# Kernel optimization log

Hardware: AMD Instinct MI355X
Metric: run time of the kernel (lower is better)

## Reference

```python
import jax, jax.numpy as jnp
import numpy as np

DIN = 1024
DOUT = 1024


def setup_inputs() -> dict:
    key = jax.random.key(0)
    kx, kq, kk, kv = jax.random.split(key, 4)
    B, T = 4, 2048
    x = jax.random.normal(kx, (B, T, DIN), dtype=jnp.float32)
    # nn.Linear weights are (dout, din); init like PyTorch default scale
    s = 1.0 / np.sqrt(DIN)
    Wq = jax.random.uniform(kq, (DOUT, DIN), minval=-s, maxval=s, dtype=jnp.float32)
    Wk = jax.random.uniform(kk, (DOUT, DIN), minval=-s, maxval=s, dtype=jnp.float32)
    Wv = jax.random.uniform(kv, (DOUT, DIN), minval=-s, maxval=s, dtype=jnp.float32)
    return {"x": x, "Wq": Wq, "Wk": Wk, "Wv": Wv}


def reference(x, Wq, Wk, Wv):
    B, T, _ = x.shape
    q = jnp.einsum('btd,ed->bte', x, Wq)
    k = jnp.einsum('btd,ed->bte', x, Wk)
    v = jnp.einsum('btd,ed->bte', x, Wv)
    attn = jnp.einsum('bqe,bke->bqk', q, k)  # [B, T, T]
    # Faithful to source: masked_fill result is discarded, so the causal mask
    # is a MULTIPLICATIVE tril of ones (upper triangle logits become 0, not -inf).
    mask = jnp.tril(jnp.ones((T, T), dtype=attn.dtype))
    attn = attn * mask
    # Faithful to source: scale by sqrt(last dim of attn) = sqrt(T), not sqrt(d).
    attn = jax.nn.softmax(attn / jnp.sqrt(jnp.asarray(T, attn.dtype)), axis=-1)
    return jnp.einsum('bqk,bke->bqe', attn, v)
```

## Files before the change

kernel.cpp:

```cpp
#include <hip/hip_runtime.h>
#include <stdint.h>

#define BB 4
#define TT 2048
#define DD 1024
#define NX (BB*TT*DD)
#define NW (DD*DD)
#define SCALE 0.022097086912079608f
#define SCALEI 2.157918643757774e-5f
#define UNSCALE 7.689469810104304e-6f
#define Q8F 2.4606299212598425e-4f
#define VQ 48.0f
#define PVF (1.0f/3072.0f)
#define TQF (1.0f/24.0f)

typedef short v8s __attribute__((ext_vector_type(8)));
typedef float v4f __attribute__((ext_vector_type(4)));
typedef int   v4i __attribute__((ext_vector_type(4)));
typedef uint8_t u8;

typedef const void __attribute__((address_space(1))) *as1_cvp;
typedef void __attribute__((address_space(3))) *as3_vp;

__device__ __forceinline__ short f2bf(float f) {
    union { float f; uint32_t u; } x; x.f = f;
    uint32_t r = x.u + 0x7fffu + ((x.u >> 16) & 1u);
    return (short)(r >> 16);
}
__device__ __forceinline__ float bf2f(short s) {
    union { uint32_t u; float f; } x; x.u = ((uint32_t)(uint16_t)s) << 16;
    return x.f;
}
__device__ __forceinline__ int bsum(uint32_t w) {
#if __has_builtin(__builtin_amdgcn_sdot4)
    return __builtin_amdgcn_sdot4((int)w, 0x01010101, 0, false);
#else
    return (int)(signed char)(w & 255) + (int)(signed char)((w >> 8) & 255) +
           (int)(signed char)((w >> 16) & 255) + (int)(signed char)((w >> 24) & 255);
#endif
}

__device__ __forceinline__ void gl_lds16(const void* g, const void* lds_wave_base) {
    __builtin_amdgcn_global_load_lds(
        (as1_cvp)(uintptr_t)g,
        (as3_vp)(uint32_t)(uintptr_t)lds_wave_base,
        16, 0, 0);
}

#define WAITV(N) asm volatile("s_waitcnt vmcnt(" #N ")" ::: "memory")

__device__ __forceinline__ void stage128B(const u8* __restrict__ g, int lda,
                                          u8* lds, int tid) {
    #pragma unroll
    for (int s = 0; s < 2; s++) {
        int t = s * 512 + tid;
        int r = t >> 3, c = t & 7, cg = c ^ (r & 7);
        gl_lds16(g + (size_t)r * lda + cg * 16, lds + s * 8192 + (tid >> 6) * 1024);
    }
}
__device__ __forceinline__ void stB8(const u8* __restrict__ g, u8* lds, int tid, int p) {
    #pragma unroll
    for (int s = 0; s < 2; s++) {
        int t = s * 512 + tid;
        int r = t >> 3, c = t & 7, cg = c ^ (r & 7);
        int grow = ((r >> 5) << 6) + p * 32 + (r & 31);
        gl_lds16(g + (size_t)grow * 1024 + cg * 16, lds + s * 8192 + (tid >> 6) * 1024);
    }
}
__device__ __forceinline__ v4i frag16(const u8* lds, int row, int c) {
    return *(const v4i*)(lds + row * 128 + ((c ^ (row & 7)) << 4));
}

__device__ __forceinline__ void stage64(const u8* __restrict__ g, u8* lds, int tid) {
    int r = tid >> 2, c = tid & 3;
    gl_lds16(g + (size_t)r * 1024 + c * 16, lds + (tid >> 6) * 1024);
}
__device__ __forceinline__ v4i fragK64(const u8* lds, int row, int gq) {
    return *(const v4i*)(lds + row * 64 + gq * 16);
}

__global__ void k_convert(const float* __restrict__ x, const float* __restrict__ Wq,
                          const float* __restrict__ Wk, const float* __restrict__ Wv,
                          u8* __restrict__ dst8, float* __restrict__ rowsum) {
    int i = blockIdx.x * 256 + threadIdx.x;
    if (i < BB * TT) rowsum[i] = (float)((15 - ((i & 2047) >> 7)) * 128);
    size_t base = (size_t)i * 4;
    const float* src; size_t off; float sc; bool clip;
    if (base < NX)               { src = x;  off = base; sc = 32.f; clip = true; }
    else if (base < NX + NW)     { src = Wq; off = base - NX; sc = 4064.f; clip = false; }
    else if (base < NX + 2*(size_t)NW) { src = Wk; off = base - NX - NW; sc = 4064.f; clip = false; }
    else                         { src = Wv; off = base - NX - 2*(size_t)NW; sc = 4064.f; clip = false; }
    float4 f = *(const float4*)(src + off);
    float a0 = f.x * sc, a1 = f.y * sc, a2 = f.z * sc, a3 = f.w * sc;
    if (clip) {
        a0 = fminf(fmaxf(a0, -127.f), 127.f);
        a1 = fminf(fmaxf(a1, -127.f), 127.f);
        a2 = fminf(fmaxf(a2, -127.f), 127.f);
        a3 = fminf(fmaxf(a3, -127.f), 127.f);
    }
    int q0 = __float2int_rn(a0), q1 = __float2int_rn(a1);
    int q2 = __float2int_rn(a2), q3 = __float2int_rn(a3);
    uint32_t w = (uint32_t)(q0 & 255) | ((uint32_t)(q1 & 255) << 8) |
                 ((uint32_t)(q2 & 255) << 16) | ((uint32_t)(q3 & 255) << 24);
    *(uint32_t*)(dst8 + base) = w;
}

__global__ __launch_bounds__(512, 2) void k_qkv(const u8* __restrict__ xb,
                                                const u8* __restrict__ wb,
                                                u8* __restrict__ q8,
                                                u8* __restrict__ k8,
                                                short* __restrict__ vt,
                                                u8* __restrict__ vt8) {
    int h = blockIdx.x;
    int w = (h & 7) * 96 + (h >> 3);
    int which = w >> 8, rem = w & 255, ntile = rem >> 6, mtile = rem & 63;
    int m0 = mtile * 128, n0 = ntile * 256;
    const u8* Ag = xb + (size_t)m0 * 1024;
    const u8* Bg = wb + (size_t)which * NW + (size_t)n0 * 1024;
    __shared__ __align__(16) u8 SH[98304];
    int tid = threadIdx.x, lane = tid & 63, wave = tid >> 6;
    int wm = wave >> 2, wn = wave & 3;
    int lr = lane & 15, lq = lane >> 4;
    int arow = wm * 64 + lr;
    int brow = wn * 32 + lr;
    v4i acc[4][4];
    #pragma unroll
    for (int i = 0; i < 4; i++)
        #pragma unroll
        for (int j = 0; j < 4; j++) acc[i][j] = (v4i){0, 0, 0, 0};

    stage128B(Ag, 1024, SH, tid);
    stB8(Bg, SH + 16384, tid, 0);
    stB8(Bg, SH + 32768, tid, 1);

    #pragma unroll
    for (int t = 0; t < 8; ++t) {
        u8* S  = SH + (t & 1) * 49152;
        u8* Sn = SH + ((t + 1) & 1) * 49152;
        const u8* Agn = Ag + (t + 1) * 128;
        const u8* Bgn = Bg + (t + 1) * 128;
        WAITV(2);
        __builtin_amdgcn_s_barrier();
        v4i af[4][2], bf[2][2];
        #pragma unroll
        for (int i = 0; i < 4; i++)
            #pragma unroll
            for (int kh = 0; kh < 2; kh++) af[i][kh] = frag16(S, arow + i * 16, kh * 4 + lq);
        #pragma unroll
        for (int jj = 0; jj < 2; jj++)
            #pragma unroll
            for (int kh = 0; kh < 2; kh++) bf[jj][kh] = frag16(S + 16384, brow + jj * 16, kh * 4 + lq);
        if (t < 7) {
            stage128B(Agn, 1024, Sn,  tid);
            stB8(Bgn, Sn + 16384, tid, 0);
        }
        __builtin_amdgcn_s_setprio(1);
        #pragma unroll
        for (int kh = 0; kh < 2; kh++)
            #pragma unroll
            for (int i = 0; i < 4; i++)
                #pragma unroll
                for (int jj = 0; jj < 2; jj++)
                    acc[i][jj] = __builtin_amdgcn_mfma_i32_16x16x64_i8(af[i][kh], bf[jj][kh], acc[i][jj], 0, 0, 0);
        __builtin_amdgcn_s_setprio(0);
        if (t < 7) { WAITV(4); }
        else       { WAITV(0); }
        __builtin_amdgcn_s_barrier();
        v4i bg2[2][2];
        #pragma unroll
        for (int jj = 0; jj < 2; jj++)
            #pragma unroll
            for (int kh = 0; kh < 2; kh++) bg2[jj][kh] = frag16(S + 32768, brow + jj * 16, kh * 4 + lq);
        if (t < 7) stB8(Bgn, Sn + 32768, tid, 1);
        __builtin_amdgcn_s_setprio(1);
        #pragma unroll
        for (int kh = 0; kh < 2; kh++)
            #pragma unroll
            for (int i = 0; i < 4; i++)
                #pragma unroll
                for (int jj = 0; jj < 2; jj++)
                    acc[i][2 + jj] = __builtin_amdgcn_mfma_i32_16x16x64_i8(af[i][kh], bg2[jj][kh], acc[i][2 + jj], 0, 0, 0);
        __builtin_amdgcn_s_setprio(0);
    }

    if (which == 2) {
        #pragma unroll
        for (int a = 0; a < 4; a++)
            #pragma unroll
            for (int b = 0; b < 4; b++) {
                int row0 = m0 + wm * 64 + a * 16 + lq * 4;
                int col  = n0 + wn * 64 + b * 16 + lr;
                int bb = row0 >> 11, tt0 = row0 & 2047;
                size_t idx = ((size_t)bb << 21) + ((size_t)col << 11) + tt0;
                float v0 = (float)acc[a][b][0] * UNSCALE;
                float v1 = (float)acc[a][b][1] * UNSCALE;
                float v2 = (float)acc[a][b][2] * UNSCALE;
                float v3 = (float)acc[a][b][3] * UNSCALE;
                short4 hv; hv.x = f2bf(v0); hv.y = f2bf(v1); hv.z = f2bf(v2); hv.w = f2bf(v3);
                *(short4*)(vt + idx) = hv;
                int c0 = __float2int_rn(fminf(fmaxf(v0 * VQ, -127.f), 127.f));
                int c1 = __float2int_rn(fminf(fmaxf(v1 * VQ, -127.f), 127.f));
                int c2 = __float2int_rn(fminf(fmaxf(v2 * VQ, -127.f), 127.f));
                int c3 = __float2int_rn(fminf(fmaxf(v3 * VQ, -127.f), 127.f));
                uint32_t pw = (uint32_t)(c0 & 255) | ((uint32_t)(c1 & 255) << 8) |
                              ((uint32_t)(c2 & 255) << 16) | ((uint32_t)(c3 & 255) << 24);
                *(uint32_t*)(vt8 + idx) = pw;
            }
    } else {
        u8* outp = (which == 0) ? q8 : k8;
        #pragma unroll
        for (int a = 0; a < 4; a++)
            #pragma unroll
            for (int b = 0; b < 4; b++)
                #pragma unroll
                for (int r = 0; r < 4; r++) {
                    int row = m0 + wm * 64 + a * 16 + lq * 4 + r;
                    int col = n0 + wn * 64 + b * 16 + lr;
                    float v = (float)acc[a][b][r] * Q8F;
                    v = fminf(fmaxf(v, -127.f), 127.f);
                    outp[(size_t)row * 1024 + col] = (u8)(__float2int_rn(v) & 255);
                }
    }
}

__global__ void k_ts1(const short* __restrict__ vt, const u8* __restrict__ vt8,
                      float* __restrict__ TSpart, float* __restrict__ TQpart) {
    int g = blockIdx.x * 256 + threadIdx.x;
    int b = g >> 14, jt = (g >> 10) & 15, e = g & 1023;
    const short* row = vt + ((size_t)b << 21) + ((size_t)e << 11) + jt * 128;
    float s = 0.f;
    #pragma unroll
    for (int c = 0; c < 16; c++) {
        uint4 u = *(const uint4*)(row + c * 8);
        const short* hp = (const short*)&u;
        #pragma unroll
        for (int z = 0; z < 8; z++) s += bf2f(hp[z]);
    }
    TSpart[g] = s;
    const u8* row8 = vt8 + ((size_t)b << 21) + ((size_t)e << 11) + jt * 128;
    int si = 0;
    #pragma unroll
    for (int c = 0; c < 8; c++) {
        uint4 u = *(const uint4*)(row8 + c * 16);
        si += bsum(u.x) + bsum(u.y) + bsum(u.z) + bsum(u.w);
    }
    TQpart[g] = (float)si;
}
__global__ void k_ts2(const float* __restrict__ TSpart, const float* __restrict__ TQpart,
                      float* __restrict__ TS, float* __restrict__ TQ) {
    int g = blockIdx.x * 256 + threadIdx.x;
    int b = g >> 10, e = g & 1023;
    float acc = 0.f;
    TS[(size_t)(b * 17 + 16) * 1024 + e] = 0.f;
    for (int jt = 15; jt >= 0; jt--) {
        acc += TSpart[(size_t)(b * 16 + jt) * 1024 + e];
        TS[(size_t)(b * 17 + jt) * 1024 + e] = acc;
    }
    float aq = 0.f;
    TQ[(size_t)(b * 17 + 0) * 1024 + e] = 0.f;
    for (int jt = 0; jt < 16; jt++) {
        aq += TQpart[(size_t)(b * 16 + jt) * 1024 + e];
        TQ[(size_t)(b * 17 + jt + 1) * 1024 + e] = aq;
    }
}

__global__ __launch_bounds__(512, 4) void k_pk(const u8* __restrict__ q8,
                                               const u8* __restrict__ k8,
                                               char* __restrict__ P8,
                                               float* __restrict__ rowsum) {
    int pidx = blockIdx.x, b = blockIdx.z;
    int qt = 0;
    while ((qt + 1) * (qt + 2) / 2 <= pidx) qt++;
    int kt = pidx - qt * (qt + 1) / 2;
    int r0 = qt * 128;
    const u8* Ag = q8 + ((size_t)b * 2048 + r0) * 1024;
    const u8* Bg = k8 + ((size_t)b * 2048 + (size_t)kt * 128) * 1024;
    __shared__ __align__(16) u8 SH[49152];
    int tid = threadIdx.x, lane = tid & 63, wave = tid >> 6;
    int wm2 = wave >> 2, wn4 = wave & 3;
    int lr = lane & 15, lq = lane >> 4;
    v4i acc[4][2];
    #pragma unroll
    for (int i = 0; i < 4; i++)
        #pragma unroll
        for (int j = 0; j < 2; j++) acc[i][j] = (v4i){0, 0, 0, 0};

    stage64(Ag,      SH,                tid);
    stage64(Bg,      SH + 8192,         tid);
    stage64(Ag + 64, SH + 16384,        tid);
    stage64(Bg + 64, SH + 16384 + 8192, tid);

    #pragma unroll
    for (int it = 0; it < 16; ++it) {
        if (it + 1 < 16) { WAITV(2); }
        else             { WAITV(0); }
        __builtin_amdgcn_s_barrier();
        if (it + 2 < 16) {
            u8* Sn = SH + ((it + 2) % 3) * 16384;
            stage64(Ag + (it + 2) * 64, Sn,        tid);
            stage64(Bg + (it + 2) * 64, Sn + 8192, tid);
        }
        const u8* S = SH + (it % 3) * 16384;
        v4i af[4], bf[2];
        #pragma unroll
        for (int i = 0; i < 4; i++) af[i] = fragK64(S, wm2 * 64 + i * 16 + lr, lq);
        #pragma unroll
        for (int j = 0; j < 2; j++) bf[j] = fragK64(S + 8192, wn4 * 32 + j * 16 + lr, lq);
        __builtin_amdgcn_s_setprio(1);
        #pragma unroll
        for (int i = 0; i < 4; i++)
            #pragma unroll
            for (int j = 0; j < 2; j++)
                acc[i][j] = __builtin_amdgcn_mfma_i32_16x16x64_i8(af[i], bf[j], acc[i][j], 0, 0, 0);
        __builtin_amdgcn_s_setprio(0);
    }
    char* Pb = P8 + ((size_t)b << 22);
    float rs[4][4];
    #pragma unroll
    for (int i = 0; i < 4; i++)
        #pragma unroll
        for (int r = 0; r < 4; r++) rs[i][r] = 0.f;
    #pragma unroll
    for (int i = 0; i < 4; i++)
        #pragma unroll
        for (int j = 0; j < 2; j++)
            #pragma unroll
            for (int r = 0; r < 4; r++) {
                int qi = r0 + wm2 * 64 + i * 16 + lq * 4 + r;
                int kj = kt * 128 + wn4 * 32 + j * 16 + lr;
                float p = (kj <= qi) ? __expf((float)acc[i][j][r] * SCALEI) : 1.0f;
                int u = __float2int_rn(fminf(p * 64.f, 255.f));
                Pb[(size_t)qi * 2048 + kj] = (char)(u - 128);
                rs[i][r] += (float)u * 0.015625f;
            }
    #pragma unroll
    for (int m = 1; m < 16; m <<= 1)
        #pragma unroll
        for (int i = 0; i < 4; i++)
            #pragma unroll
            for (int r = 0; r < 4; r++) rs[i][r] += __shfl_xor(rs[i][r], m);
    if (lr == 0)
        #pragma unroll
        for (int i = 0; i < 4; i++)
            #pragma unroll
            for (int r = 0; r < 4; r++)
                atomicAdd(&rowsum[b * 2048 + r0 + wm2 * 64 + i * 16 + lq * 4 + r], rs[i][r]);
}

__global__ __launch_bounds__(512, 2) void k_pv(const u8* __restrict__ P8,
                                               const u8* __restrict__ vt8,
                                               const float* __restrict__ rowsum,
                                               const float* __restrict__ TS,
                                               const float* __restrict__ TQ,
                                               float* __restrict__ out) {
    int et = blockIdx.x, p = blockIdx.y, b = blockIdx.z;
    const u8* Bg = vt8 + ((size_t)b << 21) + (size_t)et * 128 * 2048;
    __shared__ __align__(16) u8 SH[98304];
    int tid = threadIdx.x, lane = tid & 63, wave = tid >> 6;
    int wm2 = wave >> 2, wn4 = wave & 3;
    int lr = lane & 15, lq = lane >> 4;

    #pragma unroll
    for (int ph = 0; ph < 2; ph++) {
        int qt = ph ? p : 15 - p;
        int r0 = qt * 128;
        int iters = qt + 1;
        const u8* Ag = P8 + ((size_t)b << 22) + (size_t)r0 * 2048;
        v4i acc[4][2];
        #pragma unroll
        for (int i = 0; i < 4; i++)
            #pragma unroll
            for (int j = 0; j < 2; j++) acc[i][j] = (v4i){0, 0, 0, 0};

        stage128B(Ag, 2048, SH,         tid);
        stage128B(Bg, 2048, SH + 16384, tid);
        if (iters > 1) {
            stage128B(Ag + 128, 2048, SH + 32768,         tid);
            stage128B(Bg + 128, 2048, SH + 32768 + 16384, tid);
        }

        for (int it = 0; it < iters; ++it) {
            if (it + 1 < iters) { WAITV(4); }
            else                { WAITV(0); }
            __builtin_amdgcn_s_barrier();
            if (it + 2 < iters) {
                u8* Sn = SH + ((it + 2) % 3) * 32768;
                stage128B(Ag + (it + 2) * 128, 2048, Sn,         tid);
                stage128B(Bg + (it + 2) * 128, 2048, Sn + 16384, tid);
            }
            const u8* S = SH + (it % 3) * 32768;
            v4i af[4][2], bf[2][2];
            #pragma unroll
            for (int i = 0; i < 4; i++)
                #pragma unroll
                for (int kh = 0; kh < 2; kh++) af[i][kh] = frag16(S, wm2 * 64 + i * 16 + lr, kh * 4 + lq);
            #pragma unroll
            for (int j = 0; j < 2; j++)
                #pragma unroll
                for (int kh = 0; kh < 2; kh++) bf[j][kh] = frag16(S + 16384, wn4 * 32 + j * 16 + lr, kh * 4 + lq);
            __builtin_amdgcn_s_setprio(1);
            #pragma unroll
            for (int kh = 0; kh < 2; kh++)
                #pragma unroll
                for (int i = 0; i < 4; i++)
                    #pragma unroll
                    for (int j = 0; j < 2; j++)
                        acc[i][j] = __builtin_amdgcn_mfma_i32_16x16x64_i8(af[i][kh], bf[j][kh], acc[i][j], 0, 0, 0);
            __builtin_amdgcn_s_setprio(0);
        }
        const float* tsrow = TS + (size_t)(b * 17 + qt + 1) * 1024;
        const float* tqrow = TQ + (size_t)(b * 17 + qt + 1) * 1024;
        #pragma unroll
        for (int i = 0; i < 4; i++)
            #pragma unroll
            for (int j = 0; j < 2; j++)
                #pragma unroll
                for (int r = 0; r < 4; r++) {
                    int row = r0 + wm2 * 64 + i * 16 + lq * 4 + r;
                    int col = et * 128 + wn4 * 32 + j * 16 + lr;
                    float numer = (float)acc[i][j][r] * PVF + tqrow[col] * TQF + tsrow[col];
                    out[((size_t)(b * 2048 + row) << 10) + col] = numer / rowsum[b * 2048 + row];
                }
        __builtin_amdgcn_s_barrier();
    }
}

extern "C" void kernel_launch(void* const* d_in, const int* in_sizes, int n_in,
                              void* d_out, int out_size, void* d_ws, size_t ws_size,
                              hipStream_t stream) {
    const float* x  = (const float*)d_in[0];
    const float* Wq = (const float*)d_in[1];
    const float* Wk = (const float*)d_in[2];
    const float* Wv = (const float*)d_in[3];
    float* out = (float*)d_out;
    char* ws = (char*)d_ws;

    u8*    xb8    = (u8*)(ws + 0);
    u8*    q8     = (u8*)(ws + 11534336);
    u8*    k8     = (u8*)(ws + 19922944);
    short* vt     = (short*)(ws + 28311552);
    u8*    vt8    = (u8*)(ws + 45088768);
    char*  P8     = (char*)(ws + 53477376);
    float* rowsum = (float*)(ws + 70254592);
    float* TSpart = (float*)(ws + 70287360);
    float* TS     = (float*)(ws + 70549504);
    float* TQpart = (float*)(ws + 70828032);
    float* TQ     = (float*)(ws + 71090176);

    k_convert<<<11264, 256, 0, stream>>>(x, Wq, Wk, Wv, xb8, rowsum);
    k_qkv<<<dim3(768, 1, 1), 512, 0, stream>>>(xb8, xb8 + NX, q8, k8, vt, vt8);
    k_ts1<<<256, 256, 0, stream>>>(vt, vt8, TSpart, TQpart);
    k_ts2<<<16, 256, 0, stream>>>(TSpart, TQpart, TS, TQ);
    k_pk<<<dim3(136, 1, 4), 512, 0, stream>>>(q8, k8, P8, rowsum);
    k_pv<<<dim3(8, 8, 4), 512, 0, stream>>>((const u8*)P8, vt8, rowsum, TS, TQ, out);
}
```

Before: 204.3 us.

## Fuse V tile-sum reductions into QKV epilogue and drop bf16 V copy

Per-tile column sums of V (float and quantized int) are now computed in the k_qkv epilogue with wave shuffles and atomics, not read back by separate k_ts1/k_ts2 kernels. The bf16 transposed V buffer is no longer written. The prefix/suffix sums over tiles move into k_pv, which reduces them into shared memory per block. This removes two launches and a 16 MB bf16 write plus its re-read, at the cost of global atomics and a small serial reduction in k_pv. Float atomics make the sums order-nondeterministic.

```diff
diff --git a/kernel.cpp b/kernel.cpp
--- a/kernel.cpp
+++ b/kernel.cpp
@@ -27,18 +27,6 @@
     uint32_t r = x.u + 0x7fffu + ((x.u >> 16) & 1u);
     return (short)(r >> 16);
 }
-__device__ __forceinline__ float bf2f(short s) {
-    union { uint32_t u; float f; } x; x.u = ((uint32_t)(uint16_t)s) << 16;
-    return x.f;
-}
-__device__ __forceinline__ int bsum(uint32_t w) {
-#if __has_builtin(__builtin_amdgcn_sdot4)
-    return __builtin_amdgcn_sdot4((int)w, 0x01010101, 0, false);
-#else
-    return (int)(signed char)(w & 255) + (int)(signed char)((w >> 8) & 255) +
-           (int)(signed char)((w >> 16) & 255) + (int)(signed char)((w >> 24) & 255);
-#endif
-}
 
 __device__ __forceinline__ void gl_lds16(const void* g, const void* lds_wave_base) {
     __builtin_amdgcn_global_load_lds(
@@ -81,9 +69,11 @@
 
 __global__ void k_convert(const float* __restrict__ x, const float* __restrict__ Wq,
                           const float* __restrict__ Wk, const float* __restrict__ Wv,
-                          u8* __restrict__ dst8, float* __restrict__ rowsum) {
+                          u8* __restrict__ dst8, float* __restrict__ rowsum,
+                          float* __restrict__ TSpart, int* __restrict__ TQint) {
     int i = blockIdx.x * 256 + threadIdx.x;
     if (i < BB * TT) rowsum[i] = (float)((15 - ((i & 2047) >> 7)) * 128);
+    if (i < BB * 16 * 1024) { TSpart[i] = 0.f; TQint[i] = 0; }
     size_t base = (size_t)i * 4;
     const float* src; size_t off; float sc; bool clip;
     if (base < NX)               { src = x;  off = base; sc = 32.f; clip = true; }
@@ -109,8 +99,9 @@
                                                 const u8* __restrict__ wb,
                                                 u8* __restrict__ q8,
                                                 u8* __restrict__ k8,
-                                                short* __restrict__ vt,
-                                                u8* __restrict__ vt8) {
+                                                u8* __restrict__ vt8,
+                                                float* __restrict__ TSpart,
+                                                int* __restrict__ TQint) {
     int h = blockIdx.x;
     int w = (h & 7) * 96 + (h >> 3);
     int which = w >> 8, rem = w & 255, ntile = rem >> 6, mtile = rem & 63;
@@ -184,28 +175,37 @@
     }
 
     if (which == 2) {
-        #pragma unroll
-        for (int a = 0; a < 4; a++)
-            #pragma unroll
-            for (int b = 0; b < 4; b++) {
+        int bb = m0 >> 11, jt = (m0 & 2047) >> 7;
+        #pragma unroll
+        for (int bI = 0; bI < 4; bI++) {
+            int col = n0 + wn * 64 + bI * 16 + lr;
+            float sf = 0.f; int si = 0;
+            #pragma unroll
+            for (int a = 0; a < 4; a++) {
                 int row0 = m0 + wm * 64 + a * 16 + lq * 4;
-                int col  = n0 + wn * 64 + b * 16 + lr;
-                int bb = row0 >> 11, tt0 = row0 & 2047;
+                int tt0 = row0 & 2047;
                 size_t idx = ((size_t)bb << 21) + ((size_t)col << 11) + tt0;
-                float v0 = (float)acc[a][b][0] * UNSCALE;
-                float v1 = (float)acc[a][b][1] * UNSCALE;
-                float v2 = (float)acc[a][b][2] * UNSCALE;
-                float v3 = (float)acc[a][b][3] * UNSCALE;
-                short4 hv; hv.x = f2bf(v0); hv.y = f2bf(v1); hv.z = f2bf(v2); hv.w = f2bf(v3);
-                *(short4*)(vt + idx) = hv;
+                float v0 = (float)acc[a][bI][0] * UNSCALE;
+                float v1 = (float)acc[a][bI][1] * UNSCALE;
+                float v2 = (float)acc[a][bI][2] * UNSCALE;
+                float v3 = (float)acc[a][bI][3] * UNSCALE;
+                sf += v0 + v1 + v2 + v3;
                 int c0 = __float2int_rn(fminf(fmaxf(v0 * VQ, -127.f), 127.f));
                 int c1 = __float2int_rn(fminf(fmaxf(v1 * VQ, -127.f), 127.f));
                 int c2 = __float2int_rn(fminf(fmaxf(v2 * VQ, -127.f), 127.f));
                 int c3 = __float2int_rn(fminf(fmaxf(v3 * VQ, -127.f), 127.f));
+                si += c0 + c1 + c2 + c3;
                 uint32_t pw = (uint32_t)(c0 & 255) | ((uint32_t)(c1 & 255) << 8) |
                               ((uint32_t)(c2 & 255) << 16) | ((uint32_t)(c3 & 255) << 24);
                 *(uint32_t*)(vt8 + idx) = pw;
             }
+            sf += __shfl_xor(sf, 16); sf += __shfl_xor(sf, 32);
+            si += __shfl_xor(si, 16); si += __shfl_xor(si, 32);
+            if (lq == 0) {
+                atomicAdd(&TSpart[(size_t)(bb * 16 + jt) * 1024 + col], sf);
+                atomicAdd(&TQint[(size_t)(bb * 16 + jt) * 1024 + col], si);
+            }
+        }
     } else {
         u8* outp = (which == 0) ? q8 : k8;
         #pragma unroll
@@ -220,47 +220,6 @@
                     v = fminf(fmaxf(v, -127.f), 127.f);
                     outp[(size_t)row * 1024 + col] = (u8)(__float2int_rn(v) & 255);
                 }
-    }
-}
-
-__global__ void k_ts1(const short* __restrict__ vt, const u8* __restrict__ vt8,
-                      float* __restrict__ TSpart, float* __restrict__ TQpart) {
-    int g = blockIdx.x * 256 + threadIdx.x;
-    int b = g >> 14, jt = (g >> 10) & 15, e = g & 1023;
-    const short* row = vt + ((size_t)b << 21) + ((size_t)e << 11) + jt * 128;
-    float s = 0.f;
-    #pragma unroll
-    for (int c = 0; c < 16; c++) {
-        uint4 u = *(const uint4*)(row + c * 8);
-        const short* hp = (const short*)&u;
-        #pragma unroll
-        for (int z = 0; z < 8; z++) s += bf2f(hp[z]);
-    }
-    TSpart[g] = s;
-    const u8* row8 = vt8 + ((size_t)b << 21) + ((size_t)e << 11) + jt * 128;
-    int si = 0;
-    #pragma unroll
-    for (int c = 0; c < 8; c++) {
-        uint4 u = *(const uint4*)(row8 + c * 16);
-        si += bsum(u.x) + bsum(u.y) + bsum(u.z) + bsum(u.w);
-    }
-    TQpart[g] = (float)si;
-}
-__global__ void k_ts2(const float* __restrict__ TSpart, const float* __restrict__ TQpart,
-                      float* __restrict__ TS, float* __restrict__ TQ) {
-    int g = blockIdx.x * 256 + threadIdx.x;
-    int b = g >> 10, e = g & 1023;
-    float acc = 0.f;
-    TS[(size_t)(b * 17 + 16) * 1024 + e] = 0.f;
-    for (int jt = 15; jt >= 0; jt--) {
-        acc += TSpart[(size_t)(b * 16 + jt) * 1024 + e];
-        TS[(size_t)(b * 17 + jt) * 1024 + e] = acc;
-    }
-    float aq = 0.f;
-    TQ[(size_t)(b * 17 + 0) * 1024 + e] = 0.f;
-    for (int jt = 0; jt < 16; jt++) {
-        aq += TQpart[(size_t)(b * 16 + jt) * 1024 + e];
-        TQ[(size_t)(b * 17 + jt + 1) * 1024 + e] = aq;
     }
 }
 
@@ -350,12 +309,13 @@
 __global__ __launch_bounds__(512, 2) void k_pv(const u8* __restrict__ P8,
                                                const u8* __restrict__ vt8,
                                                const float* __restrict__ rowsum,
-                                               const float* __restrict__ TS,
-                                               const float* __restrict__ TQ,
+                                               const float* __restrict__ TSpart,
+                                               const int* __restrict__ TQint,
                                                float* __restrict__ out) {
     int et = blockIdx.x, p = blockIdx.y, b = blockIdx.z;
     const u8* Bg = vt8 + ((size_t)b << 21) + (size_t)et * 128 * 2048;
     __shared__ __align__(16) u8 SH[98304];
+    __shared__ float tsq[128], tqq[128];
     int tid = threadIdx.x, lane = tid & 63, wave = tid >> 6;
     int wm2 = wave >> 2, wn4 = wave & 3;
     int lr = lane & 15, lq = lane >> 4;
@@ -377,6 +337,16 @@
         if (iters > 1) {
             stage128B(Ag + 128, 2048, SH + 32768,         tid);
             stage128B(Bg + 128, 2048, SH + 32768 + 16384, tid);
+        }
+        if (tid < 128) {
+            int e = et * 128 + tid;
+            float ts = 0.f;
+            for (int jt = qt + 1; jt < 16; jt++) ts += TSpart[(size_t)(b * 16 + jt) * 1024 + e];
+            int tq = 0;
+            for (int jt = 0; jt <= qt; jt++) tq += TQint[(size_t)(b * 16 + jt) * 1024 + e];
+            tsq[tid] = ts;
+            tqq[tid] = (float)tq;
+            asm volatile("s_waitcnt lgkmcnt(0)" ::: "memory");
         }
 
         for (int it = 0; it < iters; ++it) {
@@ -408,8 +378,6 @@
                         acc[i][j] = __builtin_amdgcn_mfma_i32_16x16x64_i8(af[i][kh], bf[j][kh], acc[i][j], 0, 0, 0);
             __builtin_amdgcn_s_setprio(0);
         }
-        const float* tsrow = TS + (size_t)(b * 17 + qt + 1) * 1024;
-        const float* tqrow = TQ + (size_t)(b * 17 + qt + 1) * 1024;
         #pragma unroll
         for (int i = 0; i < 4; i++)
             #pragma unroll
@@ -417,8 +385,9 @@
                 #pragma unroll
                 for (int r = 0; r < 4; r++) {
                     int row = r0 + wm2 * 64 + i * 16 + lq * 4 + r;
-                    int col = et * 128 + wn4 * 32 + j * 16 + lr;
-                    float numer = (float)acc[i][j][r] * PVF + tqrow[col] * TQF + tsrow[col];
+                    int cl = wn4 * 32 + j * 16 + lr;
+                    int col = et * 128 + cl;
+                    float numer = (float)acc[i][j][r] * PVF + tqq[cl] * TQF + tsq[cl];
                     out[((size_t)(b * 2048 + row) << 10) + col] = numer / rowsum[b * 2048 + row];
                 }
         __builtin_amdgcn_s_barrier();
@@ -438,19 +407,14 @@
     u8*    xb8    = (u8*)(ws + 0);
     u8*    q8     = (u8*)(ws + 11534336);
     u8*    k8     = (u8*)(ws + 19922944);
-    short* vt     = (short*)(ws + 28311552);
-    u8*    vt8    = (u8*)(ws + 45088768);
-    char*  P8     = (char*)(ws + 53477376);
-    float* rowsum = (float*)(ws + 70254592);
-    float* TSpart = (float*)(ws + 70287360);
-    float* TS     = (float*)(ws + 70549504);
-    float* TQpart = (float*)(ws + 70828032);
-    float* TQ     = (float*)(ws + 71090176);
-
-    k_convert<<<11264, 256, 0, stream>>>(x, Wq, Wk, Wv, xb8, rowsum);
-    k_qkv<<<dim3(768, 1, 1), 512, 0, stream>>>(xb8, xb8 + NX, q8, k8, vt, vt8);
-    k_ts1<<<256, 256, 0, stream>>>(vt, vt8, TSpart, TQpart);
-    k_ts2<<<16, 256, 0, stream>>>(TSpart, TQpart, TS, TQ);
+    u8*    vt8    = (u8*)(ws + 28311552);
+    char*  P8     = (char*)(ws + 36700160);
+    float* rowsum = (float*)(ws + 53477376);
+    float* TSpart = (float*)(ws + 53510144);
+    int*   TQint  = (int*)(ws + 53772288);
+
+    k_convert<<<11264, 256, 0, stream>>>(x, Wq, Wk, Wv, xb8, rowsum, TSpart, TQint);
+    k_qkv<<<dim3(768, 1, 1), 512, 0, stream>>>(xb8, xb8 + NX, q8, k8, vt8, TSpart, TQint);
     k_pk<<<dim3(136, 1, 4), 512, 0, stream>>>(q8, k8, P8, rowsum);
-    k_pv<<<dim3(8, 8, 4), 512, 0, stream>>>((const u8*)P8, vt8, rowsum, TS, TQ, out);
-}
+    k_pv<<<dim3(8, 8, 4), 512, 0, stream>>>((const u8*)P8, vt8, rowsum, TSpart, TQint, out);
+}
```

Result: faster. 190.6 us (median of 2 runs) (-6.7%).
